# Optimization experiments

Hardware: AMD Instinct MI355X
Metric: run time of the kernel (lower is better)

## Reference

```python
import jax, jax.numpy as jnp
import numpy as np

IN_CH = 128
INTER = max(IN_CH // 8, 1)  # 16

def setup_inputs() -> dict:
    key = jax.random.key(0)
    ks = jax.random.split(key, 10)
    B, C, D, H, W = 2, IN_CH, 16, 24, 24
    s = 1.0 / np.sqrt(C)
    so = 1.0 / np.sqrt(INTER)
    return {
        "x":  jax.random.normal(ks[0], (B, C, D, H, W), dtype=jnp.float32),
        "Wq": jax.random.normal(ks[1], (INTER, C), dtype=jnp.float32) * s,
        "bq": jax.random.normal(ks[2], (INTER,), dtype=jnp.float32) * 0.01,
        "Wk": jax.random.normal(ks[3], (INTER, C), dtype=jnp.float32) * s,
        "bk": jax.random.normal(ks[4], (INTER,), dtype=jnp.float32) * 0.01,
        "Wv": jax.random.normal(ks[5], (INTER, C), dtype=jnp.float32) * s,
        "bv": jax.random.normal(ks[6], (INTER,), dtype=jnp.float32) * 0.01,
        "Wo": jax.random.normal(ks[7], (C, INTER), dtype=jnp.float32) * so,
        "bo": jax.random.normal(ks[8], (C,), dtype=jnp.float32) * 0.01,
        "gamma": jnp.zeros((1,), dtype=jnp.float32) + 0.5,  # nonzero so attn path is exercised
    }

def reference(x, Wq, bq, Wk, bk, Wv, bv, Wo, bo, gamma):
    B, C, D, H, W = x.shape
    N = D * H * W
    xf = x.reshape(B, C, N)  # flatten spatial
    # 1x1x1 conv == per-voxel channel matmul
    q = jnp.einsum('ic,bcn->bin', Wq, xf) + bq[None, :, None]  # [B,I,N]
    k = jnp.einsum('ic,bcn->bin', Wk, xf) + bk[None, :, None]
    v = jnp.einsum('ic,bcn->bin', Wv, xf) + bv[None, :, None]
    # attention[b,n,m] = sum_i q[b,i,n] k[b,i,m]; softmax over keys m
    attn = jax.nn.softmax(jnp.einsum('bin,bim->bnm', q, k), axis=-1)
    # out[b,c,n] = sum_m v[b,c,m] attn[b,n,m]
    out = jnp.einsum('bim,bnm->bin', v, attn)  # [B,I,N]
    out = jnp.einsum('ci,bin->bcn', Wo, out) + bo[None, :, None]
    out = out.reshape(B, C, D, H, W)
    return gamma[0] * out + x
```

## Files before the change

### kernel.cpp

```cpp
#include <hip/hip_runtime.h>

#define C_CH 128
#define I_CH 16
#define NVOX 9216
#define BATCH 2
#define LOG2E 1.44269504088896340736f

typedef unsigned short ushort_t;
typedef unsigned int uint_t;
typedef short bf16x8 __attribute__((ext_vector_type(8)));
typedef float f32x4 __attribute__((ext_vector_type(4)));

static __device__ inline ushort_t f2bf_rne(float x) {
    uint_t u = __builtin_bit_cast(uint_t, x);
    u = (u + 0x7FFFu + ((u >> 16) & 1u)) >> 16;
    return (ushort_t)u;
}

static __device__ inline float fast_exp2(float x) {
#if __has_builtin(__builtin_amdgcn_exp2f)
    return __builtin_amdgcn_exp2f(x);
#else
    return exp2f(x);
#endif
}

__global__ __launch_bounds__(256) void qkv_kernel(
    const float* __restrict__ x,
    const float* __restrict__ Wq, const float* __restrict__ bq,
    const float* __restrict__ Wk, const float* __restrict__ bk,
    const float* __restrict__ Wv, const float* __restrict__ bv,
    ushort_t* __restrict__ qb, ushort_t* __restrict__ kb,
    ushort_t* __restrict__ vT)
{
    __shared__ float xs[C_CH][64];
    __shared__ float ws[3][I_CH][C_CH];

    const int blk = blockIdx.x;
    const int b   = blk / (NVOX / 64);
    const int n0  = (blk % (NVOX / 64)) * 64;
    const int t   = threadIdx.x;

    {
        float4* wsq = (float4*)&ws[0][0][0];
        float4* wsk = (float4*)&ws[1][0][0];
        float4* wsv = (float4*)&ws[2][0][0];
        wsq[t]       = ((const float4*)Wq)[t];
        wsq[t + 256] = ((const float4*)Wq)[t + 256];
        wsk[t]       = ((const float4*)Wk)[t];
        wsk[t + 256] = ((const float4*)Wk)[t + 256];
        wsv[t]       = ((const float4*)Wv)[t];
        wsv[t + 256] = ((const float4*)Wv)[t + 256];
    }

    const float* xb = x + (size_t)b * C_CH * NVOX;
    #pragma unroll
    for (int rep = 0; rep < 8; ++rep) {
        int idx4 = rep * 256 + t;
        int c    = idx4 >> 4;
        int n4   = (idx4 & 15) << 2;
        *(float4*)&xs[c][n4] = *(const float4*)(xb + (size_t)c * NVOX + n0 + n4);
    }
    __syncthreads();

    const int n  = t & 63;
    const int iw = t >> 6;
    const int i0 = iw * 4;

    float aq[4] = {0.f,0.f,0.f,0.f};
    float ak[4] = {0.f,0.f,0.f,0.f};
    float av[4] = {0.f,0.f,0.f,0.f};

    #pragma unroll 2
    for (int c = 0; c < C_CH; c += 4) {
        float xv0 = xs[c + 0][n];
        float xv1 = xs[c + 1][n];
        float xv2 = xs[c + 2][n];
        float xv3 = xs[c + 3][n];
        #pragma unroll
        for (int j = 0; j < 4; ++j) {
            float4 w4;
            w4 = *(const float4*)&ws[0][i0 + j][c];
            aq[j] = fmaf(w4.x, xv0, fmaf(w4.y, xv1, fmaf(w4.z, xv2, fmaf(w4.w, xv3, aq[j]))));
            w4 = *(const float4*)&ws[1][i0 + j][c];
            ak[j] = fmaf(w4.x, xv0, fmaf(w4.y, xv1, fmaf(w4.z, xv2, fmaf(w4.w, xv3, ak[j]))));
            w4 = *(const float4*)&ws[2][i0 + j][c];
            av[j] = fmaf(w4.x, xv0, fmaf(w4.y, xv1, fmaf(w4.z, xv2, fmaf(w4.w, xv3, av[j]))));
        }
    }

    const size_t vox = (size_t)b * NVOX + n0 + n;
    ushort4 qv, kv;
    qv.x = f2bf_rne((aq[0] + bq[i0+0]) * LOG2E);
    qv.y = f2bf_rne((aq[1] + bq[i0+1]) * LOG2E);
    qv.z = f2bf_rne((aq[2] + bq[i0+2]) * LOG2E);
    qv.w = f2bf_rne((aq[3] + bq[i0+3]) * LOG2E);
    kv.x = f2bf_rne(ak[0] + bk[i0+0]); kv.y = f2bf_rne(ak[1] + bk[i0+1]);
    kv.z = f2bf_rne(ak[2] + bk[i0+2]); kv.w = f2bf_rne(ak[3] + bk[i0+3]);
    *(ushort4*)(qb + vox * I_CH + i0) = qv;
    *(ushort4*)(kb + vox * I_CH + i0) = kv;

    const int nl = n0 + n;
    #pragma unroll
    for (int j = 0; j < 4; ++j)
        vT[((size_t)b * I_CH + i0 + j) * NVOX + nl] = f2bf_rne(av[j] + bv[i0+j]);
}

__global__ __launch_bounds__(512) void attn_kernel(
    const ushort_t* __restrict__ qb, const ushort_t* __restrict__ kb,
    const ushort_t* __restrict__ vT,
    const float* __restrict__ Wo, const float* __restrict__ bo,
    const float* __restrict__ gamma, const float* __restrict__ x,
    float* __restrict__ out)
{
    __shared__ float po[4][32][18];
    __shared__ float lsh[8][33];
    __shared__ float aot[16][40];
    __shared__ float wo_s[C_CH][17];

    const int tid  = threadIdx.x;
    const int w    = tid >> 6;
    const int lane = tid & 63;
    const int l16  = lane & 15;
    const int quad = lane >> 4;

    {
        const int c  = tid >> 2;
        const int i4 = (tid & 3) * 4;
        float4 wv = *(const float4*)(Wo + c * I_CH + i4);
        wo_s[c][i4 + 0] = wv.x; wo_s[c][i4 + 1] = wv.y;
        wo_s[c][i4 + 2] = wv.z; wo_s[c][i4 + 3] = wv.w;
    }

    const int qvox0 = blockIdx.x * 32;
    const int b     = qvox0 / NVOX;
    const int nloc0 = qvox0 - b * NVOX;

    bf16x8 qf0 = (bf16x8)0, qf1 = (bf16x8)0;
    if (quad < 2) {
        qf0 = __builtin_bit_cast(bf16x8,
              *(const int4*)(qb + (size_t)(qvox0 + l16) * I_CH + quad * 8));
        qf1 = __builtin_bit_cast(bf16x8,
              *(const int4*)(qb + (size_t)(qvox0 + 16 + l16) * I_CH + quad * 8));
    }

    const int p0     = ((l16 >> 2) << 3) + (l16 & 3);
    const int mchunk = w * (NVOX / 8);
    const ushort_t* kp = kb + ((size_t)b * NVOX + mchunk + p0) * I_CH + (quad & 1) * 8;
    const ushort_t* vp = vT + ((size_t)b * I_CH + l16) * NVOX + mchunk + quad * 8;

    f32x4 O0 = {0.f,0.f,0.f,0.f}, O1 = {0.f,0.f,0.f,0.f};
    f32x4 L0 = {0.f,0.f,0.f,0.f}, L1 = {0.f,0.f,0.f,0.f};
    const f32x4 Z = {0.f,0.f,0.f,0.f};
    int4 onesi; onesi.x = onesi.y = onesi.z = onesi.w = 0x3F803F80;
    const bf16x8 ones = __builtin_bit_cast(bf16x8, onesi);

    int4 ka0 = *(const int4*)(kp);
    int4 ka1 = *(const int4*)(kp + 4 * I_CH);
    int4 va  = *(const int4*)(vp);

    #pragma unroll 2
    for (int it = 0; it < NVOX / 8 / 32; ++it) {
        kp += 32 * I_CH;
        vp += 32;
        int4 ka0n = *(const int4*)(kp);
        int4 ka1n = *(const int4*)(kp + 4 * I_CH);
        int4 van  = *(const int4*)(vp);

        f32x4 s00 = __builtin_amdgcn_mfma_f32_16x16x32_bf16(
            __builtin_bit_cast(bf16x8, ka0), qf0, Z, 0, 0, 0);
        f32x4 s01 = __builtin_amdgcn_mfma_f32_16x16x32_bf16(
            __builtin_bit_cast(bf16x8, ka1), qf0, Z, 0, 0, 0);
        f32x4 s10 = __builtin_amdgcn_mfma_f32_16x16x32_bf16(
            __builtin_bit_cast(bf16x8, ka0), qf1, Z, 0, 0, 0);
        f32x4 s11 = __builtin_amdgcn_mfma_f32_16x16x32_bf16(
            __builtin_bit_cast(bf16x8, ka1), qf1, Z, 0, 0, 0);

        {
            float p00 = fast_exp2(s00.x), p01 = fast_exp2(s00.y);
            float p02 = fast_exp2(s00.z), p03 = fast_exp2(s00.w);
            float p10 = fast_exp2(s01.x), p11 = fast_exp2(s01.y);
            float p12 = fast_exp2(s01.z), p13 = fast_exp2(s01.w);
            uint_t d0 = __builtin_amdgcn_perm(__builtin_bit_cast(uint_t, p01),
                                              __builtin_bit_cast(uint_t, p00), 0x07060302u);
            uint_t d1 = __builtin_amdgcn_perm(__builtin_bit_cast(uint_t, p03),
                                              __builtin_bit_cast(uint_t, p02), 0x07060302u);
            uint_t d2 = __builtin_amdgcn_perm(__builtin_bit_cast(uint_t, p11),
                                              __builtin_bit_cast(uint_t, p10), 0x07060302u);
            uint_t d3 = __builtin_amdgcn_perm(__builtin_bit_cast(uint_t, p13),
                                              __builtin_bit_cast(uint_t, p12), 0x07060302u);
            int4 pbi = make_int4((int)d0, (int)d1, (int)d2, (int)d3);
            bf16x8 pb = __builtin_bit_cast(bf16x8, pbi);
            O0 = __builtin_amdgcn_mfma_f32_16x16x32_bf16(
                __builtin_bit_cast(bf16x8, va), pb, O0, 0, 0, 0);
            L0 = __builtin_amdgcn_mfma_f32_16x16x32_bf16(ones, pb, L0, 0, 0, 0);
        }
        {
            float p00 = fast_exp2(s10.x), p01 = fast_exp2(s10.y);
            float p02 = fast_exp2(s10.z), p03 = fast_exp2(s10.w);
            float p10 = fast_exp2(s11.x), p11 = fast_exp2(s11.y);
            float p12 = fast_exp2(s11.z), p13 = fast_exp2(s11.w);
            uint_t d0 = __builtin_amdgcn_perm(__builtin_bit_cast(uint_t, p01),
                                              __builtin_bit_cast(uint_t, p00), 0x07060302u);
            uint_t d1 = __builtin_amdgcn_perm(__builtin_bit_cast(uint_t, p03),
                                              __builtin_bit_cast(uint_t, p02), 0x07060302u);
            uint_t d2 = __builtin_amdgcn_perm(__builtin_bit_cast(uint_t, p11),
                                              __builtin_bit_cast(uint_t, p10), 0x07060302u);
            uint_t d3 = __builtin_amdgcn_perm(__builtin_bit_cast(uint_t, p13),
                                              __builtin_bit_cast(uint_t, p12), 0x07060302u);
            int4 pbi = make_int4((int)d0, (int)d1, (int)d2, (int)d3);
            bf16x8 pb = __builtin_bit_cast(bf16x8, pbi);
            O1 = __builtin_amdgcn_mfma_f32_16x16x32_bf16(
                __builtin_bit_cast(bf16x8, va), pb, O1, 0, 0, 0);
            L1 = __builtin_amdgcn_mfma_f32_16x16x32_bf16(ones, pb, L1, 0, 0, 0);
        }

        ka0 = ka0n; ka1 = ka1n; va = van;
    }

    if (w < 4) {
        #pragma unroll
        for (int r = 0; r < 4; ++r) {
            po[w][quad * 4 + r][l16]      = O0[r];
            po[w][16 + quad * 4 + r][l16] = O1[r];
        }
    }
    if (quad == 0) { lsh[w][l16] = L0.x; lsh[w][16 + l16] = L1.x; }
    __syncthreads();

    if (w >= 4) {
        #pragma unroll
        for (int r = 0; r < 4; ++r) {
            po[w - 4][quad * 4 + r][l16]      += O0[r];
            po[w - 4][16 + quad * 4 + r][l16] += O1[r];
        }
    }
    __syncthreads();

    {
        const int q32 = tid & 31;
        const int i   = tid >> 5;
        const int row = (q32 >> 4) * 16 + i;
        const int col = q32 & 15;
        float v = 0.f, l = 0.f;
        #pragma unroll
        for (int ww = 0; ww < 4; ++ww) v += po[ww][row][col];
        #pragma unroll
        for (int ww = 0; ww < 8; ++ww) l += lsh[ww][q32];
        aot[i][q32] = v / l;
    }
    __syncthreads();

    const float g  = gamma[0];
    const int   c  = tid >> 2;
    const int   qh = (tid & 3) * 8;

    float acc[8];
    {
        const float b0 = bo[c];
        #pragma unroll
        for (int q = 0; q < 8; ++q) acc[q] = b0;
    }
    #pragma unroll
    for (int i = 0; i < 16; ++i) {
        const float wv = wo_s[c][i];
        float4 a0 = *(const float4*)&aot[i][qh];
        float4 a1 = *(const float4*)&aot[i][qh + 4];
        acc[0] = fmaf(wv, a0.x, acc[0]); acc[1] = fmaf(wv, a0.y, acc[1]);
        acc[2] = fmaf(wv, a0.z, acc[2]); acc[3] = fmaf(wv, a0.w, acc[3]);
        acc[4] = fmaf(wv, a1.x, acc[4]); acc[5] = fmaf(wv, a1.y, acc[5]);
        acc[6] = fmaf(wv, a1.z, acc[6]); acc[7] = fmaf(wv, a1.w, acc[7]);
    }

    const size_t gi = ((size_t)b * C_CH + c) * NVOX + nloc0 + qh;
    float4 x0 = *(const float4*)(x + gi);
    float4 x1 = *(const float4*)(x + gi + 4);
    float4 o0, o1;
    o0.x = fmaf(g, acc[0], x0.x); o0.y = fmaf(g, acc[1], x0.y);
    o0.z = fmaf(g, acc[2], x0.z); o0.w = fmaf(g, acc[3], x0.w);
    o1.x = fmaf(g, acc[4], x1.x); o1.y = fmaf(g, acc[5], x1.y);
    o1.z = fmaf(g, acc[6], x1.z); o1.w = fmaf(g, acc[7], x1.w);
    *(float4*)(out + gi)     = o0;
    *(float4*)(out + gi + 4) = o1;
}

extern "C" void kernel_launch(void* const* d_in, const int* in_sizes, int n_in,
                              void* d_out, int out_size, void* d_ws, size_t ws_size,
                              hipStream_t stream) {
    const float* x     = (const float*)d_in[0];
    const float* Wq    = (const float*)d_in[1];
    const float* bq    = (const float*)d_in[2];
    const float* bk    = (const float*)d_in[4];
    const float* Wk    = (const float*)d_in[3];
    const float* bv    = (const float*)d_in[6];
    const float* Wv    = (const float*)d_in[5];
    const float* Wo    = (const float*)d_in[7];
    const float* bo    = (const float*)d_in[8];
    const float* gamma = (const float*)d_in[9];
    float* out = (float*)d_out;

    ushort_t* qb = (ushort_t*)d_ws;
    ushort_t* kb = qb + (size_t)BATCH * NVOX * I_CH;
    ushort_t* vT = kb + (size_t)BATCH * NVOX * I_CH;

    hipLaunchKernelGGL(qkv_kernel, dim3(BATCH * NVOX / 64), dim3(256), 0, stream,
                       x, Wq, bq, Wk, bk, Wv, bv, qb, kb, vT);
    hipLaunchKernelGGL(attn_kernel, dim3(BATCH * NVOX / 32), dim3(512), 0, stream,
                       qb, kb, vT, Wo, bo, gamma, x, out);
}
```

Measured before the change: 129.0 us.

## Use 16x16x16 bf16 MFMA for scores and shrink QKV tiles to 16 voxels

The QK^T score product previously used 16x16x32 bf16 MFMA with half the K dimension zero-padded, since the head dimension is only 16. It now uses a 16x16x16 bf16 MFMA with 8-byte K/Q fragments, which halves score-MFMA work and the K bytes loaded per iteration. The QKV projection kernel is retiled to 16 voxels per block with one output per thread, launching four times as many blocks. That raises parallelism but adds per-block weight staging overhead, and the fallback path would pad again if the smaller MFMA builtin is missing.

```diff
diff --git a/kernel.cpp b/kernel.cpp
--- a/kernel.cpp
+++ b/kernel.cpp
@@ -8,6 +8,7 @@
 
 typedef unsigned short ushort_t;
 typedef unsigned int uint_t;
+typedef short bf16x4 __attribute__((ext_vector_type(4)));
 typedef short bf16x8 __attribute__((ext_vector_type(8)));
 typedef float f32x4 __attribute__((ext_vector_type(4)));
 
@@ -22,6 +23,21 @@
     return __builtin_amdgcn_exp2f(x);
 #else
     return exp2f(x);
+#endif
+}
+
+static __device__ inline f32x4 score_mfma(bf16x4 a, bf16x4 b, f32x4 c) {
+#if __has_builtin(__builtin_amdgcn_mfma_f32_16x16x16bf16_1k)
+    return __builtin_amdgcn_mfma_f32_16x16x16bf16_1k(a, b, c, 0, 0, 0);
+#elif __has_builtin(__builtin_amdgcn_mfma_f32_16x16x16_bf16)
+    return __builtin_amdgcn_mfma_f32_16x16x16_bf16(a, b, c, 0, 0, 0);
+#else
+    int2 ai = __builtin_bit_cast(int2, a);
+    int2 bi = __builtin_bit_cast(int2, b);
+    int4 a4 = make_int4(ai.x, ai.y, 0, 0);
+    int4 b4 = make_int4(bi.x, bi.y, 0, 0);
+    return __builtin_amdgcn_mfma_f32_16x16x32_bf16(
+        __builtin_bit_cast(bf16x8, a4), __builtin_bit_cast(bf16x8, b4), c, 0, 0, 0);
 #endif
 }
 
@@ -33,77 +49,59 @@
     ushort_t* __restrict__ qb, ushort_t* __restrict__ kb,
     ushort_t* __restrict__ vT)
 {
-    __shared__ float xs[C_CH][64];
-    __shared__ float ws[3][I_CH][C_CH];
-
-    const int blk = blockIdx.x;
-    const int b   = blk / (NVOX / 64);
-    const int n0  = (blk % (NVOX / 64)) * 64;
-    const int t   = threadIdx.x;
-
-    {
-        float4* wsq = (float4*)&ws[0][0][0];
-        float4* wsk = (float4*)&ws[1][0][0];
-        float4* wsv = (float4*)&ws[2][0][0];
-        wsq[t]       = ((const float4*)Wq)[t];
-        wsq[t + 256] = ((const float4*)Wq)[t + 256];
-        wsk[t]       = ((const float4*)Wk)[t];
-        wsk[t + 256] = ((const float4*)Wk)[t + 256];
-        wsv[t]       = ((const float4*)Wv)[t];
-        wsv[t + 256] = ((const float4*)Wv)[t + 256];
-    }
-
-    const float* xb = x + (size_t)b * C_CH * NVOX;
-    #pragma unroll
-    for (int rep = 0; rep < 8; ++rep) {
-        int idx4 = rep * 256 + t;
-        int c    = idx4 >> 4;
-        int n4   = (idx4 & 15) << 2;
-        *(float4*)&xs[c][n4] = *(const float4*)(xb + (size_t)c * NVOX + n0 + n4);
+    __shared__ float ws[3][I_CH][132];
+    __shared__ float xs[C_CH][I_CH];
+
+    const int t    = threadIdx.x;
+    const int vox0 = blockIdx.x * 16;
+    const int b    = vox0 / NVOX;
+    const int n0   = vox0 - b * NVOX;
+
+    {
+        const int i  = t >> 4;
+        const int c8 = (t & 15) * 8;
+        const float4* wq4 = (const float4*)(Wq + i * C_CH + c8);
+        const float4* wk4 = (const float4*)(Wk + i * C_CH + c8);
+        const float4* wv4 = (const float4*)(Wv + i * C_CH + c8);
+        *(float4*)&ws[0][i][c8]     = wq4[0];
+        *(float4*)&ws[0][i][c8 + 4] = wq4[1];
+        *(float4*)&ws[1][i][c8]     = wk4[0];
+        *(float4*)&ws[1][i][c8 + 4] = wk4[1];
+        *(float4*)&ws[2][i][c8]     = wv4[0];
+        *(float4*)&ws[2][i][c8 + 4] = wv4[1];
+    }
+
+    {
+        const float* xb = x + (size_t)b * C_CH * NVOX + n0;
+        const int c   = t >> 2;
+        const int col = (t & 3) * 4;
+        *(float4*)&xs[c][col]      = *(const float4*)(xb + (size_t)c * NVOX + col);
+        *(float4*)&xs[c + 64][col] = *(const float4*)(xb + (size_t)(c + 64) * NVOX + col);
     }
     __syncthreads();
 
-    const int n  = t & 63;
-    const int iw = t >> 6;
-    const int i0 = iw * 4;
-
-    float aq[4] = {0.f,0.f,0.f,0.f};
-    float ak[4] = {0.f,0.f,0.f,0.f};
-    float av[4] = {0.f,0.f,0.f,0.f};
-
-    #pragma unroll 2
+    const int n = t & 15;
+    const int i = t >> 4;
+
+    float aq = 0.f, ak = 0.f, av = 0.f;
+    #pragma unroll 4
     for (int c = 0; c < C_CH; c += 4) {
-        float xv0 = xs[c + 0][n];
-        float xv1 = xs[c + 1][n];
-        float xv2 = xs[c + 2][n];
-        float xv3 = xs[c + 3][n];
-        #pragma unroll
-        for (int j = 0; j < 4; ++j) {
-            float4 w4;
-            w4 = *(const float4*)&ws[0][i0 + j][c];
-            aq[j] = fmaf(w4.x, xv0, fmaf(w4.y, xv1, fmaf(w4.z, xv2, fmaf(w4.w, xv3, aq[j]))));
-            w4 = *(const float4*)&ws[1][i0 + j][c];
-            ak[j] = fmaf(w4.x, xv0, fmaf(w4.y, xv1, fmaf(w4.z, xv2, fmaf(w4.w, xv3, ak[j]))));
-            w4 = *(const float4*)&ws[2][i0 + j][c];
-            av[j] = fmaf(w4.x, xv0, fmaf(w4.y, xv1, fmaf(w4.z, xv2, fmaf(w4.w, xv3, av[j]))));
-        }
-    }
-
-    const size_t vox = (size_t)b * NVOX + n0 + n;
-    ushort4 qv, kv;
-    qv.x = f2bf_rne((aq[0] + bq[i0+0]) * LOG2E);
-    qv.y = f2bf_rne((aq[1] + bq[i0+1]) * LOG2E);
-    qv.z = f2bf_rne((aq[2] + bq[i0+2]) * LOG2E);
-    qv.w = f2bf_rne((aq[3] + bq[i0+3]) * LOG2E);
-    kv.x = f2bf_rne(ak[0] + bk[i0+0]); kv.y = f2bf_rne(ak[1] + bk[i0+1]);
-    kv.z = f2bf_rne(ak[2] + bk[i0+2]); kv.w = f2bf_rne(ak[3] + bk[i0+3]);
-    *(ushort4*)(qb + vox * I_CH + i0) = qv;
-    *(ushort4*)(kb + vox * I_CH + i0) = kv;
-
-    const int nl = n0 + n;
-    #pragma unroll
-    for (int j = 0; j < 4; ++j)
-        vT[((size_t)b * I_CH + i0 + j) * NVOX + nl] = f2bf_rne(av[j] + bv[i0+j]);
+        float x0 = xs[c + 0][n];
+        float x1 = xs[c + 1][n];
+        float x2 = xs[c + 2][n];
+        float x3 = xs[c + 3][n];
+        float4 wq = *(const float4*)&ws[0][i][c];
+        float4 wk = *(const float4*)&ws[1][i][c];
+        float4 wv = *(const float4*)&ws[2][i][c];
+        aq = fmaf(wq.x, x0, fmaf(wq.y, x1, fmaf(wq.z, x2, fmaf(wq.w, x3, aq))));
+        ak = fmaf(wk.x, x0, fmaf(wk.y, x1, fmaf(wk.z, x2, fmaf(wk.w, x3, ak))));
+        av = fmaf(wv.x, x0, fmaf(wv.y, x1, fmaf(wv.z, x2, fmaf(wv.w, x3, av))));
+    }
+
+    const size_t vox = (size_t)vox0 + n;
+    qb[vox * I_CH + i] = f2bf_rne((aq + bq[i]) * LOG2E);
+    kb[vox * I_CH + i] = f2bf_rne(ak + bk[i]);
+    vT[((size_t)b * I_CH + i) * NVOX + n0 + n] = f2bf_rne(av + bv[i]);
 }
 
 __global__ __launch_bounds__(512) void attn_kernel(
@@ -136,17 +134,14 @@
     const int b     = qvox0 / NVOX;
     const int nloc0 = qvox0 - b * NVOX;
 
-    bf16x8 qf0 = (bf16x8)0, qf1 = (bf16x8)0;
-    if (quad < 2) {
-        qf0 = __builtin_bit_cast(bf16x8,
-              *(const int4*)(qb + (size_t)(qvox0 + l16) * I_CH + quad * 8));
-        qf1 = __builtin_bit_cast(bf16x8,
-              *(const int4*)(qb + (size_t)(qvox0 + 16 + l16) * I_CH + quad * 8));
-    }
+    bf16x4 qf0 = __builtin_bit_cast(bf16x4,
+        *(const int2*)(qb + (size_t)(qvox0 + l16) * I_CH + quad * 4));
+    bf16x4 qf1 = __builtin_bit_cast(bf16x4,
+        *(const int2*)(qb + (size_t)(qvox0 + 16 + l16) * I_CH + quad * 4));
 
     const int p0     = ((l16 >> 2) << 3) + (l16 & 3);
     const int mchunk = w * (NVOX / 8);
-    const ushort_t* kp = kb + ((size_t)b * NVOX + mchunk + p0) * I_CH + (quad & 1) * 8;
+    const ushort_t* kp = kb + ((size_t)b * NVOX + mchunk + p0) * I_CH + quad * 4;
     const ushort_t* vp = vT + ((size_t)b * I_CH + l16) * NVOX + mchunk + quad * 8;
 
     f32x4 O0 = {0.f,0.f,0.f,0.f}, O1 = {0.f,0.f,0.f,0.f};
@@ -155,26 +150,24 @@
     int4 onesi; onesi.x = onesi.y = onesi.z = onesi.w = 0x3F803F80;
     const bf16x8 ones = __builtin_bit_cast(bf16x8, onesi);
 
-    int4 ka0 = *(const int4*)(kp);
-    int4 ka1 = *(const int4*)(kp + 4 * I_CH);
+    int2 ka0 = *(const int2*)(kp);
+    int2 ka1 = *(const int2*)(kp + 4 * I_CH);
     int4 va  = *(const int4*)(vp);
 
     #pragma unroll 2
     for (int it = 0; it < NVOX / 8 / 32; ++it) {
         kp += 32 * I_CH;
         vp += 32;
-        int4 ka0n = *(const int4*)(kp);
-        int4 ka1n = *(const int4*)(kp + 4 * I_CH);
+        int2 ka0n = *(const int2*)(kp);
+        int2 ka1n = *(const int2*)(kp + 4 * I_CH);
         int4 van  = *(const int4*)(vp);
 
-        f32x4 s00 = __builtin_amdgcn_mfma_f32_16x16x32_bf16(
-            __builtin_bit_cast(bf16x8, ka0), qf0, Z, 0, 0, 0);
-        f32x4 s01 = __builtin_amdgcn_mfma_f32_16x16x32_bf16(
-            __builtin_bit_cast(bf16x8, ka1), qf0, Z, 0, 0, 0);
-        f32x4 s10 = __builtin_amdgcn_mfma_f32_16x16x32_bf16(
-            __builtin_bit_cast(bf16x8, ka0), qf1, Z, 0, 0, 0);
-        f32x4 s11 = __builtin_amdgcn_mfma_f32_16x16x32_bf16(
-            __builtin_bit_cast(bf16x8, ka1), qf1, Z, 0, 0, 0);
+        bf16x4 kA0 = __builtin_bit_cast(bf16x4, ka0);
+        bf16x4 kA1 = __builtin_bit_cast(bf16x4, ka1);
+        f32x4 s00 = score_mfma(kA0, qf0, Z);
+        f32x4 s01 = score_mfma(kA1, qf0, Z);
+        f32x4 s10 = score_mfma(kA0, qf1, Z);
+        f32x4 s11 = score_mfma(kA1, qf1, Z);
 
         {
             float p00 = fast_exp2(s00.x), p01 = fast_exp2(s00.y);
@@ -290,10 +283,10 @@
     const float* x     = (const float*)d_in[0];
     const float* Wq    = (const float*)d_in[1];
     const float* bq    = (const float*)d_in[2];
+    const float* Wk    = (const float*)d_in[3];
     const float* bk    = (const float*)d_in[4];
-    const float* Wk    = (const float*)d_in[3];
+    const float* Wv    = (const float*)d_in[5];
     const float* bv    = (const float*)d_in[6];
-    const float* Wv    = (const float*)d_in[5];
     const float* Wo    = (const float*)d_in[7];
     const float* bo    = (const float*)d_in[8];
     const float* gamma = (const float*)d_in[9];
@@ -303,7 +296,7 @@
     ushort_t* kb = qb + (size_t)BATCH * NVOX * I_CH;
     ushort_t* vT = kb + (size_t)BATCH * NVOX * I_CH;
 
-    hipLaunchKernelGGL(qkv_kernel, dim3(BATCH * NVOX / 64), dim3(256), 0, stream,
+    hipLaunchKernelGGL(qkv_kernel, dim3(BATCH * NVOX / 16), dim3(256), 0, stream,
                        x, Wq, bq, Wk, bk, Wv, bv, qb, kb, vT);
     hipLaunchKernelGGL(attn_kernel, dim3(BATCH * NVOX / 32), dim3(512), 0, stream,
                        qb, kb, vT, Wo, bo, gamma, x, out);
```

Result: no change. 127.9 us (-0.9%).
